# Kernel optimization log

Measured on AMD Instinct MI355X. Metric: run time of the kernel, lower is better.

The kernel has to match this reference:

```python
import jax, jax.numpy as jnp
import numpy as np

B, T, I, H = 64, 512, 512, 1024  # batch, seq_len, input_size, hidden_size
G = 4 * H  # LSTM gate size


def setup_inputs() -> dict:
    key = jax.random.key(0)
    ks = jax.random.split(key, 9)
    s = 1.0 / np.sqrt(H)  # reset_parameters: uniform(-1/sqrt(H), 1/sqrt(H))
    u = lambda k, shape: jax.random.uniform(k, shape, jnp.float32, -s, s)
    return dict(
        x=jax.random.normal(ks[0], (B, T, I), jnp.float32),
        w_ih0=u(ks[1], (G, I)), w_hh0=u(ks[2], (G, H)),
        b_ih0=u(ks[3], (G,)), b_hh0=u(ks[4], (G,)),
        w_ih1=u(ks[5], (G, H)), w_hh1=u(ks[6], (G, H)),
        b_ih1=u(ks[7], (G,)), b_hh1=u(ks[8], (G,)),
        m_ih0=jnp.ones((G, I), bool), m_hh0=jnp.ones((G, H), bool),
        m_ih1=jnp.ones((G, H), bool), m_hh1=jnp.ones((G, H), bool),
    )


def _lstm_layer(x_tm, w_ih, w_hh, b_ih, b_hh, m_ih, m_hh):
    # x_tm: [T, B, in]; masked weights computed ONCE (the torch loop recomputes per step)
    wi = (w_ih * m_ih).T  # [in, 4H]
    wh = (w_hh * m_hh).T  # [H, 4H]
    Hh = w_hh.shape[1]
    h0 = jnp.zeros((x_tm.shape[1], Hh), x_tm.dtype)

    def step(carry, xt):
        h, c = carry
        gates = xt @ wi + b_ih + h @ wh + b_hh  # [B, 4H]
        i, f, g, o = jnp.split(gates, 4, axis=-1)  # chunk order: input, forget, cell, out
        c = jax.nn.sigmoid(f) * c + jax.nn.sigmoid(i) * jnp.tanh(g)
        h = jax.nn.sigmoid(o) * jnp.tanh(c)
        return (h, c), h

    _, ys = jax.lax.scan(step, (h0, h0), x_tm)
    return ys  # [T, B, H]


def reference(x, w_ih0, w_hh0, b_ih0, b_hh0, w_ih1, w_hh1, b_ih1, b_hh1,
              m_ih0, m_hh0, m_ih1, m_hh1):
    xt = jnp.swapaxes(x, 0, 1)  # time-major [T, B, I]
    y0 = _lstm_layer(xt, w_ih0, w_hh0, b_ih0, b_hh0, m_ih0, m_hh0)
    y1 = _lstm_layer(y0, w_ih1, w_hh1, b_ih1, b_hh1, m_ih1, m_hh1)
    return y1[-1]  # last timestep hidden of final layer: [B, H]
```

## Files before the change

### kernel.cpp

```cpp
#include <hip/hip_runtime.h>
#include <hip/hip_bf16.h>


#define B_ 64
#define T_ 512
#define I_ 512
#define H_ 1024
#define SH 65536

typedef __attribute__((ext_vector_type(8))) short short8;
typedef __attribute__((ext_vector_type(4))) float f32x4;

static __device__ __forceinline__ ushort f2bf(float f) {
  __hip_bfloat16 h = __float2bfloat16(f);
  return *reinterpret_cast<ushort*>(&h);
}
static __device__ __forceinline__ float sigm(float v) {
  return 1.0f / (1.0f + expf(-v));
}
static __device__ __forceinline__ void store16_wt(void* p, f32x4 v) {
  asm volatile("global_store_dwordx4 %0, %1, off sc0 sc1" : : "v"(p), "v"(v) : "memory");
}
template <typename T>
static __device__ __forceinline__ void pinv(T& x) {
  asm volatile("" : "+v"(x));
}
static __device__ __forceinline__ void poll8(int* base, int lane) {
  while (1) {
    int v = __hip_atomic_load(base + (lane & 7) * 16, __ATOMIC_RELAXED,
                              __HIP_MEMORY_SCOPE_AGENT);
    if (__all(v >= 16)) break;
    __builtin_amdgcn_s_sleep(2);
  }
}

__global__ void prep_x(const float* __restrict__ x, ushort* __restrict__ xtm, long n) {
  long idx = (long)blockIdx.x * blockDim.x + threadIdx.x;
  long stride = (long)gridDim.x * blockDim.x;
  for (; idx < n; idx += stride) {
    int i = (int)(idx % I_);
    long r = idx / I_;
    int b = (int)(r % B_);
    int t = (int)(r / B_);
    xtm[idx] = f2bf(x[(long)b * (T_ * I_) + (long)t * I_ + i]);
  }
}

__global__ void init_cnt(int* __restrict__ c, int n) {
  int i = blockIdx.x * blockDim.x + threadIdx.x;
  if (i < n) c[i] = 0;
}

#define MFMA16 __builtin_amdgcn_mfma_f32_16x16x32_bf16

template <int LAYER>
static __device__ __forceinline__ void run_layer(
    const ushort* __restrict__ xtm, ushort* __restrict__ y0, ushort* __restrict__ y1,
    int* __restrict__ cnt0, int* __restrict__ cnt1,
    const float* __restrict__ wih, const float* __restrict__ whh,
    const float* __restrict__ bih, const float* __restrict__ bhh,
    float* __restrict__ out, int sub, float* accx, ushort* hbuf) {
  constexpr int K0 = LAYER ? H_ : I_;
  constexpr int NF = LAYER ? 8 : 6;

  const int hbase = sub * 8;
  const int tid = threadIdx.x;
  const int lane = tid & 63, wid = tid >> 6;
  const int l15 = lane & 15, khi = lane >> 4;

  short8 breg[2][NF];
#pragma unroll
  for (int cf = 0; cf < 2; ++cf)
#pragma unroll
    for (int jj = 0; jj < NF; ++jj) {
      int kcat;
      if (LAYER == 0)
        kcat = (jj < 2) ? (2 * wid + jj) * 32 : 512 + (4 * wid + jj - 2) * 32;
      else
        kcat = (jj < 4) ? (4 * wid + jj) * 32 : 1024 + (4 * wid + jj - 4) * 32;
      kcat += khi * 8;
      const int c = cf * 16 + l15;
      const int grow = (c >> 3) * H_ + hbase + (c & 7);
      const float* src = (kcat < K0) ? (wih + (long)grow * K0 + kcat)
                                     : (whh + (long)grow * H_ + (kcat - K0));
      float4 f0 = *(const float4*)src;
      float4 f1 = *(const float4*)(src + 4);
      short8 bv;
      bv[0] = (short)f2bf(f0.x); bv[1] = (short)f2bf(f0.y);
      bv[2] = (short)f2bf(f0.z); bv[3] = (short)f2bf(f0.w);
      bv[4] = (short)f2bf(f1.x); bv[5] = (short)f2bf(f1.y);
      bv[6] = (short)f2bf(f1.z); bv[7] = (short)f2bf(f1.w);
      breg[cf][jj] = bv;
    }
#pragma unroll
  for (int cf = 0; cf < 2; ++cf)
#pragma unroll
    for (int jj = 0; jj < NF; ++jj) pinv(breg[cf][jj]);

  const int brow = tid >> 3, hc = tid & 7;
  float bs[4];
#pragma unroll
  for (int g = 0; g < 4; ++g)
    bs[g] = bih[g * H_ + hbase + hc] + bhh[g * H_ + hbase + hc];
  float creg = 0.0f;

  int* cntMy = LAYER ? cnt1 : cnt0;
  ushort* ymine = LAYER ? y1 : y0;

  for (int t = 0; t < T_; ++t) {
    f32x4 acc[4][2] = {};

    if (LAYER == 0) {
      {
        short8 a[2][4];
        const ushort* px = xtm + (long)t * (B_ * I_) + khi * 8;
#pragma unroll
        for (int jj = 0; jj < 2; ++jj)
#pragma unroll
          for (int mt = 0; mt < 4; ++mt)
            a[jj][mt] = *(const short8*)(px + (long)(mt * 16 + l15) * I_ +
                                         (2 * wid + jj) * 32);
        __builtin_amdgcn_sched_barrier(0);
#pragma unroll
        for (int jj = 0; jj < 2; ++jj)
#pragma unroll
          for (int mt = 0; mt < 4; ++mt) {
            acc[mt][0] = MFMA16(a[jj][mt], breg[0][jj], acc[mt][0], 0, 0, 0);
            acc[mt][1] = MFMA16(a[jj][mt], breg[1][jj], acc[mt][1], 0, 0, 0);
          }
      }
      if (wid == 7 && t > 0) poll8(cnt0 + (long)(t - 1) * 128, lane);
      __syncthreads();
      if (t > 0) {
        short8 a[4][4];
        const ushort* ph = y0 + (long)(t - 1) * SH;
#pragma unroll
        for (int jj = 0; jj < 4; ++jj)
#pragma unroll
          for (int mt = 0; mt < 4; ++mt) {
            const int slice = (4 * wid + jj) * 4 + khi;
            a[jj][mt] = *(const short8*)(ph + ((long)slice * 64 + mt * 16 + l15) * 8);
          }
        __builtin_amdgcn_sched_barrier(0);
#pragma unroll
        for (int jj = 0; jj < 4; ++jj)
#pragma unroll
          for (int mt = 0; mt < 4; ++mt) {
            acc[mt][0] = MFMA16(a[jj][mt], breg[0][jj + 2], acc[mt][0], 0, 0, 0);
            acc[mt][1] = MFMA16(a[jj][mt], breg[1][jj + 2], acc[mt][1], 0, 0, 0);
          }
      }
    } else {
      if (t > 0) {
        if (wid == 7) poll8(cnt1 + (long)(t - 1) * 128, lane);
        __syncthreads();
        short8 a[4][4];
        const ushort* ph = y1 + (long)(t - 1) * SH;
#pragma unroll
        for (int jj = 0; jj < 4; ++jj)
#pragma unroll
          for (int mt = 0; mt < 4; ++mt) {
            const int slice = (4 * wid + jj) * 4 + khi;
            a[jj][mt] = *(const short8*)(ph + ((long)slice * 64 + mt * 16 + l15) * 8);
          }
        __builtin_amdgcn_sched_barrier(0);
#pragma unroll
        for (int jj = 0; jj < 4; ++jj)
#pragma unroll
          for (int mt = 0; mt < 4; ++mt) {
            acc[mt][0] = MFMA16(a[jj][mt], breg[0][jj + 4], acc[mt][0], 0, 0, 0);
            acc[mt][1] = MFMA16(a[jj][mt], breg[1][jj + 4], acc[mt][1], 0, 0, 0);
          }
      }
      if (wid == 7) poll8(cnt0 + (long)t * 128, lane);
      __syncthreads();
      {
        short8 a[4][4];
        const ushort* pa = y0 + (long)t * SH;
#pragma unroll
        for (int jj = 0; jj < 4; ++jj)
#pragma unroll
          for (int mt = 0; mt < 4; ++mt) {
            const int slice = (4 * wid + jj) * 4 + khi;
            a[jj][mt] = *(const short8*)(pa + ((long)slice * 64 + mt * 16 + l15) * 8);
          }
        __builtin_amdgcn_sched_barrier(0);
#pragma unroll
        for (int jj = 0; jj < 4; ++jj)
#pragma unroll
          for (int mt = 0; mt < 4; ++mt) {
            acc[mt][0] = MFMA16(a[jj][mt], breg[0][jj], acc[mt][0], 0, 0, 0);
            acc[mt][1] = MFMA16(a[jj][mt], breg[1][jj], acc[mt][1], 0, 0, 0);
          }
      }
    }

#pragma unroll
    for (int mt = 0; mt < 4; ++mt)
#pragma unroll
      for (int cf = 0; cf < 2; ++cf)
        *(f32x4*)&accx[(((wid * 4 + mt) * 32) + (cf * 16 + l15)) * 20 + khi * 4] =
            acc[mt][cf];
    __syncthreads();

    {
      const int mt2 = brow >> 4, rr = brow & 15;
      float gv[4];
#pragma unroll
      for (int g = 0; g < 4; ++g) {
        const int c = g * 8 + hc;
        float s = bs[g];
#pragma unroll
        for (int w = 0; w < 8; ++w)
          s += accx[((w * 4 + mt2) * 32 + c) * 20 + rr];
        gv[g] = s;
      }
      float cn = sigm(gv[1]) * creg + sigm(gv[0]) * tanhf(gv[2]);
      float hn = sigm(gv[3]) * tanhf(cn);
      creg = cn;
      hbuf[tid] = f2bf(hn);
      if (LAYER == 1 && t == T_ - 1) out[(long)brow * H_ + hbase + hc] = hn;
    }
    __syncthreads();

    if (wid == 0) {
      f32x4 v = *(const f32x4*)&hbuf[lane * 8];
      store16_wt(ymine + (long)t * SH + sub * 512 + lane * 8, v);
      asm volatile("s_waitcnt vmcnt(0)" ::: "memory");
      if (lane == 0) atomicAdd(cntMy + (long)t * 128 + (sub & 7) * 16, 1);
    }
  }
}

__global__ __launch_bounds__(512, 2) void lstm_persist(
    const ushort* __restrict__ xtm, ushort* __restrict__ y0, ushort* __restrict__ y1,
    int* __restrict__ cnt,
    const float* __restrict__ wih0, const float* __restrict__ whh0,
    const float* __restrict__ bih0, const float* __restrict__ bhh0,
    const float* __restrict__ wih1, const float* __restrict__ whh1,
    const float* __restrict__ bih1, const float* __restrict__ bhh1,
    float* __restrict__ out) {
  __shared__ float accx[8 * 4 * 32 * 20];
  __shared__ alignas(16) ushort hbuf[512];
  const int wg = blockIdx.x;
  int* cnt0 = cnt;
  int* cnt1 = cnt + (long)T_ * 128;
  if (wg < 128)
    run_layer<0>(xtm, y0, y1, cnt0, cnt1, wih0, whh0, bih0, bhh0, out, wg, accx, hbuf);
  else
    run_layer<1>(xtm, y0, y1, cnt0, cnt1, wih1, whh1, bih1, bhh1, out, wg - 128,
                 accx, hbuf);
}

extern "C" void kernel_launch(void* const* d_in, const int* in_sizes, int n_in,
                              void* d_out, int out_size, void* d_ws, size_t ws_size,
                              hipStream_t stream) {
  const float* x    = (const float*)d_in[0];
  const float* wih0 = (const float*)d_in[1];
  const float* whh0 = (const float*)d_in[2];
  const float* bih0 = (const float*)d_in[3];
  const float* bhh0 = (const float*)d_in[4];
  const float* wih1 = (const float*)d_in[5];
  const float* whh1 = (const float*)d_in[6];
  const float* bih1 = (const float*)d_in[7];
  const float* bhh1 = (const float*)d_in[8];

  const long szX = (long)B_ * T_ * I_ * 2;
  const long szY = (long)T_ * SH * 2;

  char* p = (char*)d_ws;
  ushort* xtm = (ushort*)p;  p += szX;
  ushort* y0  = (ushort*)p;  p += szY;
  ushort* y1  = (ushort*)p;  p += szY;
  int*    cnt = (int*)p;
  float* outp = (float*)d_out;

  prep_x<<<2048, 256, 0, stream>>>(x, xtm, (long)B_ * T_ * I_);
  init_cnt<<<512, 256, 0, stream>>>(cnt, 2 * T_ * 128);

  void* args[] = {
    (void*)&xtm, (void*)&y0, (void*)&y1, (void*)&cnt,
    (void*)&wih0, (void*)&whh0, (void*)&bih0, (void*)&bhh0,
    (void*)&wih1, (void*)&whh1, (void*)&bih1, (void*)&bhh1,
    (void*)&outp,
  };
  hipLaunchCooperativeKernel((const void*)lstm_persist, dim3(256), dim3(512),
                             args, 0, stream);
}
```

Measured before the change: 2.831 ms.

## Replace block-wide polling with per-wave counter polls and direct global h stores

Each wave now polls only the counter for the 16 producer workgroups whose h slice it reads, instead of one wave polling all eight counters and then a __syncthreads. Counter grouping changes from sub&7 to sub>>4 to match. Hidden state is stored straight to global memory with per-thread write-through short stores, dropping the LDS staging buffer. Layer 1 now consumes the layer-0 input before its own recurrent input, and launch bounds move to one block per SIMD. The aim is to shorten the inter-step critical path, at the cost of more polling traffic and many narrow global stores.

```diff
diff --git a/kernel.cpp b/kernel.cpp
--- a/kernel.cpp
+++ b/kernel.cpp
@@ -18,20 +18,17 @@
 static __device__ __forceinline__ float sigm(float v) {
   return 1.0f / (1.0f + expf(-v));
 }
-static __device__ __forceinline__ void store16_wt(void* p, f32x4 v) {
-  asm volatile("global_store_dwordx4 %0, %1, off sc0 sc1" : : "v"(p), "v"(v) : "memory");
+static __device__ __forceinline__ void store_short_wt(ushort* p, ushort v) {
+  uint w = v;
+  asm volatile("global_store_short %0, %1, off sc0 sc1" : : "v"(p), "v"(w) : "memory");
 }
 template <typename T>
 static __device__ __forceinline__ void pinv(T& x) {
   asm volatile("" : "+v"(x));
 }
-static __device__ __forceinline__ void poll8(int* base, int lane) {
-  while (1) {
-    int v = __hip_atomic_load(base + (lane & 7) * 16, __ATOMIC_RELAXED,
-                              __HIP_MEMORY_SCOPE_AGENT);
-    if (__all(v >= 16)) break;
-    __builtin_amdgcn_s_sleep(2);
-  }
+static __device__ __forceinline__ void poll1(int* p) {
+  while (__hip_atomic_load(p, __ATOMIC_RELAXED, __HIP_MEMORY_SCOPE_AGENT) < 16)
+    __builtin_amdgcn_s_sleep(1);
 }
 
 __global__ void prep_x(const float* __restrict__ x, ushort* __restrict__ xtm, long n) {
@@ -59,7 +56,7 @@
     int* __restrict__ cnt0, int* __restrict__ cnt1,
     const float* __restrict__ wih, const float* __restrict__ whh,
     const float* __restrict__ bih, const float* __restrict__ bhh,
-    float* __restrict__ out, int sub, float* accx, ushort* hbuf) {
+    float* __restrict__ out, int sub, float* accx) {
   constexpr int K0 = LAYER ? H_ : I_;
   constexpr int NF = LAYER ? 8 : 6;
 
@@ -104,8 +101,9 @@
     bs[g] = bih[g * H_ + hbase + hc] + bhh[g * H_ + hbase + hc];
   float creg = 0.0f;
 
+  ushort* ymine = LAYER ? y1 : y0;
   int* cntMy = LAYER ? cnt1 : cnt0;
-  ushort* ymine = LAYER ? y1 : y0;
+  const int relOff = (sub >> 4) * 16;
 
   for (int t = 0; t < T_; ++t) {
     f32x4 acc[4][2] = {};
@@ -120,6 +118,10 @@
           for (int mt = 0; mt < 4; ++mt)
             a[jj][mt] = *(const short8*)(px + (long)(mt * 16 + l15) * I_ +
                                          (2 * wid + jj) * 32);
+#pragma unroll
+        for (int jj = 0; jj < 2; ++jj)
+#pragma unroll
+          for (int mt = 0; mt < 4; ++mt) pinv(a[jj][mt]);
         __builtin_amdgcn_sched_barrier(0);
 #pragma unroll
         for (int jj = 0; jj < 2; ++jj)
@@ -129,9 +131,8 @@
             acc[mt][1] = MFMA16(a[jj][mt], breg[1][jj], acc[mt][1], 0, 0, 0);
           }
       }
-      if (wid == 7 && t > 0) poll8(cnt0 + (long)(t - 1) * 128, lane);
-      __syncthreads();
       if (t > 0) {
+        poll1(cnt0 + (long)(t - 1) * 128 + wid * 16);
         short8 a[4][4];
         const ushort* ph = y0 + (long)(t - 1) * SH;
 #pragma unroll
@@ -141,6 +142,10 @@
             const int slice = (4 * wid + jj) * 4 + khi;
             a[jj][mt] = *(const short8*)(ph + ((long)slice * 64 + mt * 16 + l15) * 8);
           }
+#pragma unroll
+        for (int jj = 0; jj < 4; ++jj)
+#pragma unroll
+          for (int mt = 0; mt < 4; ++mt) pinv(a[jj][mt]);
         __builtin_amdgcn_sched_barrier(0);
 #pragma unroll
         for (int jj = 0; jj < 4; ++jj)
@@ -151,29 +156,7 @@
           }
       }
     } else {
-      if (t > 0) {
-        if (wid == 7) poll8(cnt1 + (long)(t - 1) * 128, lane);
-        __syncthreads();
-        short8 a[4][4];
-        const ushort* ph = y1 + (long)(t - 1) * SH;
-#pragma unroll
-        for (int jj = 0; jj < 4; ++jj)
-#pragma unroll
-          for (int mt = 0; mt < 4; ++mt) {
-            const int slice = (4 * wid + jj) * 4 + khi;
-            a[jj][mt] = *(const short8*)(ph + ((long)slice * 64 + mt * 16 + l15) * 8);
-          }
-        __builtin_amdgcn_sched_barrier(0);
-#pragma unroll
-        for (int jj = 0; jj < 4; ++jj)
-#pragma unroll
-          for (int mt = 0; mt < 4; ++mt) {
-            acc[mt][0] = MFMA16(a[jj][mt], breg[0][jj + 4], acc[mt][0], 0, 0, 0);
-            acc[mt][1] = MFMA16(a[jj][mt], breg[1][jj + 4], acc[mt][1], 0, 0, 0);
-          }
-      }
-      if (wid == 7) poll8(cnt0 + (long)t * 128, lane);
-      __syncthreads();
+      poll1(cnt0 + (long)t * 128 + wid * 16);
       {
         short8 a[4][4];
         const ushort* pa = y0 + (long)t * SH;
@@ -184,6 +167,10 @@
             const int slice = (4 * wid + jj) * 4 + khi;
             a[jj][mt] = *(const short8*)(pa + ((long)slice * 64 + mt * 16 + l15) * 8);
           }
+#pragma unroll
+        for (int jj = 0; jj < 4; ++jj)
+#pragma unroll
+          for (int mt = 0; mt < 4; ++mt) pinv(a[jj][mt]);
         __builtin_amdgcn_sched_barrier(0);
 #pragma unroll
         for (int jj = 0; jj < 4; ++jj)
@@ -191,6 +178,30 @@
           for (int mt = 0; mt < 4; ++mt) {
             acc[mt][0] = MFMA16(a[jj][mt], breg[0][jj], acc[mt][0], 0, 0, 0);
             acc[mt][1] = MFMA16(a[jj][mt], breg[1][jj], acc[mt][1], 0, 0, 0);
+          }
+      }
+      if (t > 0) {
+        poll1(cnt1 + (long)(t - 1) * 128 + wid * 16);
+        short8 a[4][4];
+        const ushort* ph = y1 + (long)(t - 1) * SH;
+#pragma unroll
+        for (int jj = 0; jj < 4; ++jj)
+#pragma unroll
+          for (int mt = 0; mt < 4; ++mt) {
+            const int slice = (4 * wid + jj) * 4 + khi;
+            a[jj][mt] = *(const short8*)(ph + ((long)slice * 64 + mt * 16 + l15) * 8);
+          }
+#pragma unroll
+        for (int jj = 0; jj < 4; ++jj)
+#pragma unroll
+          for (int mt = 0; mt < 4; ++mt) pinv(a[jj][mt]);
+        __builtin_amdgcn_sched_barrier(0);
+#pragma unroll
+        for (int jj = 0; jj < 4; ++jj)
+#pragma unroll
+          for (int mt = 0; mt < 4; ++mt) {
+            acc[mt][0] = MFMA16(a[jj][mt], breg[0][jj + 4], acc[mt][0], 0, 0, 0);
+            acc[mt][1] = MFMA16(a[jj][mt], breg[1][jj + 4], acc[mt][1], 0, 0, 0);
           }
       }
     }
@@ -218,21 +229,16 @@
       float cn = sigm(gv[1]) * creg + sigm(gv[0]) * tanhf(gv[2]);
       float hn = sigm(gv[3]) * tanhf(cn);
       creg = cn;
-      hbuf[tid] = f2bf(hn);
+      store_short_wt(ymine + (long)t * SH + sub * 512 + tid, f2bf(hn));
       if (LAYER == 1 && t == T_ - 1) out[(long)brow * H_ + hbase + hc] = hn;
     }
+    asm volatile("s_waitcnt vmcnt(0)" ::: "memory");
     __syncthreads();
-
-    if (wid == 0) {
-      f32x4 v = *(const f32x4*)&hbuf[lane * 8];
-      store16_wt(ymine + (long)t * SH + sub * 512 + lane * 8, v);
-      asm volatile("s_waitcnt vmcnt(0)" ::: "memory");
-      if (lane == 0) atomicAdd(cntMy + (long)t * 128 + (sub & 7) * 16, 1);
-    }
+    if (tid == 0) atomicAdd(cntMy + (long)t * 128 + relOff, 1);
   }
 }
 
-__global__ __launch_bounds__(512, 2) void lstm_persist(
+__global__ __launch_bounds__(512, 1) void lstm_persist(
     const ushort* __restrict__ xtm, ushort* __restrict__ y0, ushort* __restrict__ y1,
     int* __restrict__ cnt,
     const float* __restrict__ wih0, const float* __restrict__ whh0,
@@ -241,15 +247,14 @@
     const float* __restrict__ bih1, const float* __restrict__ bhh1,
     float* __restrict__ out) {
   __shared__ float accx[8 * 4 * 32 * 20];
-  __shared__ alignas(16) ushort hbuf[512];
   const int wg = blockIdx.x;
   int* cnt0 = cnt;
   int* cnt1 = cnt + (long)T_ * 128;
   if (wg < 128)
-    run_layer<0>(xtm, y0, y1, cnt0, cnt1, wih0, whh0, bih0, bhh0, out, wg, accx, hbuf);
+    run_layer<0>(xtm, y0, y1, cnt0, cnt1, wih0, whh0, bih0, bhh0, out, wg, accx);
   else
     run_layer<1>(xtm, y0, y1, cnt0, cnt1, wih1, whh1, bih1, bhh1, out, wg - 128,
-                 accx, hbuf);
+                 accx);
 }
 
 extern "C" void kernel_launch(void* const* d_in, const int* in_sizes, int n_in,
```

After: 2.920 ms. 1.03x slower.

## Replace counter-based step sync with flag bits embedded in ring-buffered hidden data

Applied to the files above, without the earlier changes.

Removes the per-timestep atomic counters and the wave-7 polling plus __syncthreads barrier. Each consumer wave now polls the hidden-state data itself: the low bit of each bf16 pair carries a pass-pattern flag that encodes the timestep epoch. The y buffers become a 128-slot ring, and layer 0 waits on a per-block progress array written by layer 1 before it overwrites a slot. The aim is to cut synchronization latency on the serial recurrence path and shrink the workspace. The cost is bf16 mantissa corruption from the flag bits, busy polling with uncached reloads, and a tighter layer-0/layer-1 coupling through the ring.

```diff
diff --git a/kernel.cpp b/kernel.cpp
--- a/kernel.cpp
+++ b/kernel.cpp
@@ -7,9 +7,12 @@
 #define I_ 512
 #define H_ 1024
 #define SH 65536
+#define RING 128
 
 typedef __attribute__((ext_vector_type(8))) short short8;
 typedef __attribute__((ext_vector_type(4))) float f32x4;
+typedef __attribute__((ext_vector_type(4))) unsigned int u32x4;
+typedef unsigned int u32;
 
 static __device__ __forceinline__ ushort f2bf(float f) {
   __hip_bfloat16 h = __float2bfloat16(f);
@@ -18,20 +21,16 @@
 static __device__ __forceinline__ float sigm(float v) {
   return 1.0f / (1.0f + expf(-v));
 }
-static __device__ __forceinline__ void store16_wt(void* p, f32x4 v) {
-  asm volatile("global_store_dwordx4 %0, %1, off sc0 sc1" : : "v"(p), "v"(v) : "memory");
+static __device__ __forceinline__ void store_int_wt(int* p, int v) {
+  asm volatile("global_store_dword %0, %1, off sc0 sc1" : : "v"(p), "v"(v) : "memory");
 }
 template <typename T>
 static __device__ __forceinline__ void pinv(T& x) {
   asm volatile("" : "+v"(x));
 }
-static __device__ __forceinline__ void poll8(int* base, int lane) {
-  while (1) {
-    int v = __hip_atomic_load(base + (lane & 7) * 16, __ATOMIC_RELAXED,
-                              __HIP_MEMORY_SCOPE_AGENT);
-    if (__all(v >= 16)) break;
-    __builtin_amdgcn_s_sleep(2);
-  }
+static __device__ __forceinline__ u32 passpat(int tau) {
+  const int p = (tau >> 7) & 3;
+  return p == 0 ? 0x00000001u : p == 1 ? 0x00010000u : p == 2 ? 0x00010001u : 0u;
 }
 
 __global__ void prep_x(const float* __restrict__ x, ushort* __restrict__ xtm, long n) {
@@ -46,17 +45,60 @@
   }
 }
 
-__global__ void init_cnt(int* __restrict__ c, int n) {
-  int i = blockIdx.x * blockDim.x + threadIdx.x;
-  if (i < n) c[i] = 0;
+__global__ void init_zero(u32* __restrict__ a, long n) {
+  long i = (long)blockIdx.x * blockDim.x + threadIdx.x;
+  long stride = (long)gridDim.x * blockDim.x;
+  for (; i < n; i += stride) a[i] = 0;
 }
 
 #define MFMA16 __builtin_amdgcn_mfma_f32_16x16x32_bf16
+
+#define CONSUME_T(YB, TAU, JB)                                                   \
+  {                                                                              \
+    const u32 exq = passpat(TAU);                                                \
+    const ushort* yb_ = (YB) + (long)((TAU) & (RING - 1)) * SH;                  \
+    u32x4 q[4][4];                                                               \
+    _Pragma("unroll") for (int jj = 0; jj < 4; ++jj) {                           \
+      const int slice_ = (4 * wid + jj) * 4 + khi;                               \
+      _Pragma("unroll") for (int mt = 0; mt < 4; ++mt)                           \
+        q[jj][mt] =                                                              \
+            *(const u32x4*)(yb_ + (long)slice_ * 512 + (mt * 16 + l15) * 8);     \
+    }                                                                            \
+    _Pragma("unroll") for (int jj = 0; jj < 4; ++jj) {                           \
+      const int slice_ = (4 * wid + jj) * 4 + khi;                               \
+      const ushort* ab_ = yb_ + (long)slice_ * 512 + l15 * 8;                    \
+      while (1) {                                                                \
+        u32 bad = 0;                                                             \
+        _Pragma("unroll") for (int mt = 0; mt < 4; ++mt)                         \
+          _Pragma("unroll") for (int j = 0; j < 4; ++j)                          \
+            bad |= (q[jj][mt][j] & 0x00010001u) ^ exq;                           \
+        if (__all(bad == 0)) break;                                              \
+        __builtin_amdgcn_s_sleep(2);                                             \
+        _Pragma("unroll") for (int mt = 0; mt < 4; ++mt) {                       \
+          u32x4 r_;                                                              \
+          asm volatile(                                                          \
+              "global_load_dwordx4 %0, %1, off sc0 sc1\n\ts_waitcnt vmcnt(0)"    \
+              : "=&v"(r_)                                                        \
+              : "v"(ab_ + mt * 128)                                              \
+              : "memory");                                                       \
+          q[jj][mt] = r_;                                                        \
+        }                                                                        \
+        __builtin_amdgcn_sched_barrier(0);                                       \
+      }                                                                          \
+    }                                                                            \
+    __builtin_amdgcn_sched_barrier(0);                                           \
+    _Pragma("unroll") for (int jj = 0; jj < 4; ++jj)                             \
+      _Pragma("unroll") for (int mt = 0; mt < 4; ++mt) {                         \
+        short8 av_ = *(short8*)&q[jj][mt];                                       \
+        acc[mt][0] = MFMA16(av_, breg[0][jj + (JB)], acc[mt][0], 0, 0, 0);       \
+        acc[mt][1] = MFMA16(av_, breg[1][jj + (JB)], acc[mt][1], 0, 0, 0);       \
+      }                                                                          \
+  }
 
 template <int LAYER>
 static __device__ __forceinline__ void run_layer(
     const ushort* __restrict__ xtm, ushort* __restrict__ y0, ushort* __restrict__ y1,
-    int* __restrict__ cnt0, int* __restrict__ cnt1,
+    int* __restrict__ prog,
     const float* __restrict__ wih, const float* __restrict__ whh,
     const float* __restrict__ bih, const float* __restrict__ bhh,
     float* __restrict__ out, int sub, float* accx, ushort* hbuf) {
@@ -104,7 +146,6 @@
     bs[g] = bih[g * H_ + hbase + hc] + bhh[g * H_ + hbase + hc];
   float creg = 0.0f;
 
-  int* cntMy = LAYER ? cnt1 : cnt0;
   ushort* ymine = LAYER ? y1 : y0;
 
   for (int t = 0; t < T_; ++t) {
@@ -120,6 +161,10 @@
           for (int mt = 0; mt < 4; ++mt)
             a[jj][mt] = *(const short8*)(px + (long)(mt * 16 + l15) * I_ +
                                          (2 * wid + jj) * 32);
+#pragma unroll
+        for (int jj = 0; jj < 2; ++jj)
+#pragma unroll
+          for (int mt = 0; mt < 4; ++mt) pinv(a[jj][mt]);
         __builtin_amdgcn_sched_barrier(0);
 #pragma unroll
         for (int jj = 0; jj < 2; ++jj)
@@ -129,70 +174,11 @@
             acc[mt][1] = MFMA16(a[jj][mt], breg[1][jj], acc[mt][1], 0, 0, 0);
           }
       }
-      if (wid == 7 && t > 0) poll8(cnt0 + (long)(t - 1) * 128, lane);
-      __syncthreads();
-      if (t > 0) {
-        short8 a[4][4];
-        const ushort* ph = y0 + (long)(t - 1) * SH;
-#pragma unroll
-        for (int jj = 0; jj < 4; ++jj)
-#pragma unroll
-          for (int mt = 0; mt < 4; ++mt) {
-            const int slice = (4 * wid + jj) * 4 + khi;
-            a[jj][mt] = *(const short8*)(ph + ((long)slice * 64 + mt * 16 + l15) * 8);
-          }
-        __builtin_amdgcn_sched_barrier(0);
-#pragma unroll
-        for (int jj = 0; jj < 4; ++jj)
-#pragma unroll
-          for (int mt = 0; mt < 4; ++mt) {
-            acc[mt][0] = MFMA16(a[jj][mt], breg[0][jj + 2], acc[mt][0], 0, 0, 0);
-            acc[mt][1] = MFMA16(a[jj][mt], breg[1][jj + 2], acc[mt][1], 0, 0, 0);
-          }
-      }
+      if (t > 0) CONSUME_T(y0, t - 1, 2);
     } else {
-      if (t > 0) {
-        if (wid == 7) poll8(cnt1 + (long)(t - 1) * 128, lane);
-        __syncthreads();
-        short8 a[4][4];
-        const ushort* ph = y1 + (long)(t - 1) * SH;
-#pragma unroll
-        for (int jj = 0; jj < 4; ++jj)
-#pragma unroll
-          for (int mt = 0; mt < 4; ++mt) {
-            const int slice = (4 * wid + jj) * 4 + khi;
-            a[jj][mt] = *(const short8*)(ph + ((long)slice * 64 + mt * 16 + l15) * 8);
-          }
-        __builtin_amdgcn_sched_barrier(0);
-#pragma unroll
-        for (int jj = 0; jj < 4; ++jj)
-#pragma unroll
-          for (int mt = 0; mt < 4; ++mt) {
-            acc[mt][0] = MFMA16(a[jj][mt], breg[0][jj + 4], acc[mt][0], 0, 0, 0);
-            acc[mt][1] = MFMA16(a[jj][mt], breg[1][jj + 4], acc[mt][1], 0, 0, 0);
-          }
-      }
-      if (wid == 7) poll8(cnt0 + (long)t * 128, lane);
-      __syncthreads();
-      {
-        short8 a[4][4];
-        const ushort* pa = y0 + (long)t * SH;
-#pragma unroll
-        for (int jj = 0; jj < 4; ++jj)
-#pragma unroll
-          for (int mt = 0; mt < 4; ++mt) {
-            const int slice = (4 * wid + jj) * 4 + khi;
-            a[jj][mt] = *(const short8*)(pa + ((long)slice * 64 + mt * 16 + l15) * 8);
-          }
-        __builtin_amdgcn_sched_barrier(0);
-#pragma unroll
-        for (int jj = 0; jj < 4; ++jj)
-#pragma unroll
-          for (int mt = 0; mt < 4; ++mt) {
-            acc[mt][0] = MFMA16(a[jj][mt], breg[0][jj], acc[mt][0], 0, 0, 0);
-            acc[mt][1] = MFMA16(a[jj][mt], breg[1][jj], acc[mt][1], 0, 0, 0);
-          }
-      }
+      if (t > 0) CONSUME_T(y1, t - 1, 4);
+      CONSUME_T(y0, t, 0);
+      if (tid == 0) store_int_wt(prog + sub * 16, t + 1);
     }
 
 #pragma unroll
@@ -224,17 +210,33 @@
     __syncthreads();
 
     if (wid == 0) {
-      f32x4 v = *(const f32x4*)&hbuf[lane * 8];
-      store16_wt(ymine + (long)t * SH + sub * 512 + lane * 8, v);
-      asm volatile("s_waitcnt vmcnt(0)" ::: "memory");
-      if (lane == 0) atomicAdd(cntMy + (long)t * 128 + (sub & 7) * 16, 1);
+      if (LAYER == 0 && t >= RING - 1) {
+        const int need = t - RING + 2;
+        int* p1 = prog + lane * 16;
+        int* p2 = prog + (64 + lane) * 16;
+        while (1) {
+          int v1 = __hip_atomic_load(p1, __ATOMIC_RELAXED, __HIP_MEMORY_SCOPE_AGENT);
+          int v2 = __hip_atomic_load(p2, __ATOMIC_RELAXED, __HIP_MEMORY_SCOPE_AGENT);
+          if (__all(v1 >= need && v2 >= need)) break;
+          __builtin_amdgcn_s_sleep(8);
+        }
+      }
+      const u32 exq = passpat(t);
+      u32x4 qh = *(const u32x4*)&hbuf[lane * 8];
+#pragma unroll
+      for (int j = 0; j < 4; ++j) qh[j] = (qh[j] & ~0x00010001u) | exq;
+      ushort* dst = ymine + (long)(t & (RING - 1)) * SH + sub * 512 + lane * 8;
+      asm volatile("global_store_dwordx4 %0, %1, off sc0 sc1"
+                   :
+                   : "v"(dst), "v"(qh)
+                   : "memory");
     }
   }
 }
 
-__global__ __launch_bounds__(512, 2) void lstm_persist(
+__global__ __launch_bounds__(512, 1) void lstm_persist(
     const ushort* __restrict__ xtm, ushort* __restrict__ y0, ushort* __restrict__ y1,
-    int* __restrict__ cnt,
+    int* __restrict__ prog,
     const float* __restrict__ wih0, const float* __restrict__ whh0,
     const float* __restrict__ bih0, const float* __restrict__ bhh0,
     const float* __restrict__ wih1, const float* __restrict__ whh1,
@@ -243,13 +245,11 @@
   __shared__ float accx[8 * 4 * 32 * 20];
   __shared__ alignas(16) ushort hbuf[512];
   const int wg = blockIdx.x;
-  int* cnt0 = cnt;
-  int* cnt1 = cnt + (long)T_ * 128;
   if (wg < 128)
-    run_layer<0>(xtm, y0, y1, cnt0, cnt1, wih0, whh0, bih0, bhh0, out, wg, accx, hbuf);
+    run_layer<0>(xtm, y0, y1, prog, wih0, whh0, bih0, bhh0, out, wg, accx, hbuf);
   else
-    run_layer<1>(xtm, y0, y1, cnt0, cnt1, wih1, whh1, bih1, bhh1, out, wg - 128,
-                 accx, hbuf);
+    run_layer<1>(xtm, y0, y1, prog, wih1, whh1, bih1, bhh1, out, wg - 128, accx,
+                 hbuf);
 }
 
 extern "C" void kernel_launch(void* const* d_in, const int* in_sizes, int n_in,
@@ -266,20 +266,21 @@
   const float* bhh1 = (const float*)d_in[8];
 
   const long szX = (long)B_ * T_ * I_ * 2;
-  const long szY = (long)T_ * SH * 2;
+  const long szR = (long)RING * SH * 2;
+  const long szP = 128 * 16 * 4;
 
   char* p = (char*)d_ws;
-  ushort* xtm = (ushort*)p;  p += szX;
-  ushort* y0  = (ushort*)p;  p += szY;
-  ushort* y1  = (ushort*)p;  p += szY;
-  int*    cnt = (int*)p;
+  ushort* xtm  = (ushort*)p;  p += szX;
+  ushort* y0   = (ushort*)p;  p += szR;
+  ushort* y1   = (ushort*)p;  p += szR;
+  int*    prog = (int*)p;     p += szP;
   float* outp = (float*)d_out;
 
   prep_x<<<2048, 256, 0, stream>>>(x, xtm, (long)B_ * T_ * I_);
-  init_cnt<<<512, 256, 0, stream>>>(cnt, 2 * T_ * 128);
+  init_zero<<<2048, 256, 0, stream>>>((u32*)y0, (2 * szR + szP) / 4);
 
   void* args[] = {
-    (void*)&xtm, (void*)&y0, (void*)&y1, (void*)&cnt,
+    (void*)&xtm, (void*)&y0, (void*)&y1, (void*)&prog,
     (void*)&wih0, (void*)&whh0, (void*)&bih0, (void*)&bhh0,
     (void*)&wih1, (void*)&whh1, (void*)&bih1, (void*)&bhh1,
     (void*)&outp,
```

Result: slower. 4.632 ms (+63.6%).
